# Kernel optimization log

Hardware: AMD Instinct MI355X
Metric: run time of the kernel (lower is better)

The kernel has to match this reference:

```python
import jax, jax.numpy as jnp
import numpy as np

D_MODEL = 1024
N_HEADS = 16
HEAD_DIM = D_MODEL // N_HEADS
B, T = 4, 2048


def setup_inputs() -> dict:
    key = jax.random.key(0)
    k1, k2, k3, k4 = jax.random.split(key, 4)
    x = jax.random.normal(k1, (B, T, D_MODEL), dtype=jnp.float32)
    # bool key-padding mask: True = masked (padded) position
    pad_mask = jax.random.randint(k2, (B, T), 0, 2).astype(jnp.bool_)
    # torch Linear weights: [out_features, in_features], bias=False
    W_qkv = jax.random.normal(k3, (3 * D_MODEL, D_MODEL), dtype=jnp.float32) * (1.0 / np.sqrt(D_MODEL))
    W_proj = jax.random.normal(k4, (D_MODEL, D_MODEL), dtype=jnp.float32) * (1.0 / np.sqrt(D_MODEL))
    return {"x": x, "pad_mask": pad_mask, "W_qkv": W_qkv, "W_proj": W_proj}


def reference(x, pad_mask, W_qkv, W_proj):
    Bv, Tv, C = x.shape
    H, Dh = N_HEADS, HEAD_DIM
    # qkv projection: x @ W_qkv.T -> [B,T,3C], reshape to [B,T,3,H,Dh]
    qkv = jnp.einsum('btc,oc->bto', x, W_qkv).reshape(Bv, Tv, 3, H, Dh)
    q = jnp.transpose(qkv[:, :, 0], (0, 2, 1, 3))  # [B,H,T,Dh]
    k = jnp.transpose(qkv[:, :, 1], (0, 2, 1, 3))
    v = jnp.transpose(qkv[:, :, 2], (0, 2, 1, 3))
    scale = 1.0 / jnp.sqrt(jnp.asarray(Dh, x.dtype))
    attn = jnp.einsum('bhqd,bhkd->bhqk', q, k) * scale  # [B,H,T,T]
    # key-padding mask: broadcast [B,1,1,T]
    attn = jnp.where(pad_mask[:, None, None, :], -jnp.inf, attn)
    attn = jax.nn.softmax(attn, axis=-1)
    out = jnp.einsum('bhqk,bhkd->bhqd', attn, v)  # [B,H,T,Dh]
    out = jnp.transpose(out, (0, 2, 1, 3)).reshape(Bv, Tv, C)
    return jnp.einsum('btc,oc->bto', out, W_proj)
```

## Files before the change

kernel.cpp:

```cpp
#include <hip/hip_runtime.h>
#include <hip/hip_bf16.h>
#include <stdint.h>

typedef __bf16 bf16_t;
typedef __bf16 bf16x8 __attribute__((ext_vector_type(8)));
typedef __bf16 bf16x4 __attribute__((ext_vector_type(4)));
typedef float f32x4 __attribute__((ext_vector_type(4)));

#define DEVFN static __device__ __forceinline__

DEVFN f32x4 mfma16(bf16x8 a, bf16x8 b, f32x4 c) {
  return __builtin_amdgcn_mfma_f32_16x16x32_bf16(a, b, c, 0, 0, 0);
}

#define GLL16(gsrc, ldst) __builtin_amdgcn_global_load_lds( \
    (__attribute__((address_space(1))) void*)(gsrc), \
    (__attribute__((address_space(3))) void*)(ldst), 16, 0, 0)

#define SCALE_Q 0.1803368801111204f

__global__ void prep(const float* __restrict__ x, const float* __restrict__ wqkv,
                     const float* __restrict__ wproj, bf16_t* __restrict__ xb,
                     bf16_t* __restrict__ wqkvb, bf16_t* __restrict__ wprojb,
                     const int* __restrict__ mask, int* __restrict__ tc,
                     int* __restrict__ nk, bf16_t* __restrict__ kb,
                     bf16_t* __restrict__ vtb) {
  const int tid = threadIdx.x;
  if (blockIdx.x < 12288) {
    const int i = blockIdx.x * 256 + tid;
    const float* s;
    bf16_t* d;
    int off;
    if (i < 2097152) { s = x; d = xb; off = i; }
    else if (i < 2097152 + 786432) { s = wqkv; d = wqkvb; off = i - 2097152; }
    else { s = wproj; d = wprojb; off = i - 2883584; }
    f32x4 v = reinterpret_cast<const f32x4*>(s)[off];
    bf16x4 o;
    o[0] = (bf16_t)v[0]; o[1] = (bf16_t)v[1]; o[2] = (bf16_t)v[2]; o[3] = (bf16_t)v[3];
    reinterpret_cast<bf16x4*>(d)[off] = o;
    return;
  }
  const int b = blockIdx.x - 12288;
  const int lane = tid & 63, wv = tid >> 6;
  __shared__ int nk_s;
  const int* mrow = mask + b * 2048;
  if (wv == 0) {
    int base = 0;
    for (int cs = 0; cs < 2048; cs += 64) {
      const int mval = mrow[cs + lane];
      const unsigned long long bal = __ballot(mval == 0);
      const int pre = __popcll(bal & ((1ull << lane) - 1ull));
      if (!mval) tc[b * 2048 + base + pre] = cs + lane;
      base += __popcll(bal);
    }
    if (lane == 0) nk_s = base;
  }
  __syncthreads();
  const int nkb = nk_s;
  if (tid == 0) nk[b] = nkb;
  for (int i = nkb + tid; i < 2048; i += 256) tc[b * 2048 + i] = -1;
  const int ce = (nkb + 63) & ~63;
  for (int hh = wv; hh < 16; hh += 4) {
    const size_t bh = (size_t)(b * 16 + hh);
    for (int r = nkb; r < ce; ++r) {
      kb[(bh * 2048 + r) * 64 + lane] = (bf16_t)0.f;
      vtb[(bh * 64 + lane) * 2048 + r] = (bf16_t)0.f;
    }
  }
}

template <int EPI>
__global__ __launch_bounds__(256, 2)
void gemm_ct(const bf16_t* __restrict__ A, const bf16_t* __restrict__ Bx,
             bf16_t* __restrict__ qb, bf16_t* __restrict__ kb,
             bf16_t* __restrict__ vtb, float* __restrict__ fout,
             const int* __restrict__ tc, const int* __restrict__ nkp) {
  constexpr int K = 1024;
  __shared__ alignas(16) unsigned short At[128 * 64];
  __shared__ alignas(16) unsigned short Bt[128 * 64];
  const int tid = threadIdx.x;
  const int lane = tid & 63, w = tid >> 6;
  const int c = lane & 15, g = lane >> 4;
  const int oBase = blockIdx.x * 128, mBase = blockIdx.y * 128;
  const int wo = (w >> 1) * 64, wm = (w & 1) * 64;

  int nkb = 0;
  bool kv = false;
  if (EPI == 0) {
    nkb = nkp[mBase >> 11];
    kv = (blockIdx.x >= 8);
    if (kv && (mBase & 2047) >= nkb) return;
  }
  int brow[4];
#pragma unroll
  for (int i = 0; i < 4; ++i) {
    const int r = (i * 4 + w) * 8 + (lane >> 3);
    if (EPI == 0 && kv) {
      const int t = tc[(mBase >> 11) * 2048 + (mBase & 2047) + r];
      brow[i] = (mBase & ~2047) + (t < 0 ? 0 : t);
    } else {
      brow[i] = mBase + r;
    }
  }

  f32x4 acc[4][4] = {};

  for (int k0 = 0; k0 < K; k0 += 64) {
#pragma unroll
    for (int i = 0; i < 4; ++i) {
      const int cid = (i * 4 + w) * 64 + lane;
      const int r = cid >> 3;
      const int ss = (cid & 7) ^ (r & 7);
      GLL16(A + (size_t)(oBase + r) * K + k0 + ss * 8, &At[(i * 4 + w) * 512]);
      GLL16(Bx + (size_t)brow[i] * K + k0 + ss * 8, &Bt[(i * 4 + w) * 512]);
    }
    __syncthreads();
    bf16x8 af[4][2], bfr[4][2];
#pragma unroll
    for (int f = 0; f < 4; ++f) {
#pragma unroll
      for (int kc = 0; kc < 2; ++kc) {
        const int ra = wo + f * 16 + c;
        af[f][kc] = *reinterpret_cast<const bf16x8*>(&At[ra * 64 + ((kc * 4 + g) ^ (ra & 7)) * 8]);
        const int rb = wm + f * 16 + c;
        bfr[f][kc] = *reinterpret_cast<const bf16x8*>(&Bt[rb * 64 + ((kc * 4 + g) ^ (rb & 7)) * 8]);
      }
    }
    __builtin_amdgcn_s_setprio(1);
#pragma unroll
    for (int of = 0; of < 4; ++of)
#pragma unroll
      for (int mf = 0; mf < 4; ++mf)
#pragma unroll
        for (int kc = 0; kc < 2; ++kc)
          acc[of][mf] = mfma16(af[of][kc], bfr[mf][kc], acc[of][mf]);
    __builtin_amdgcn_s_setprio(0);
    __syncthreads();
  }

#pragma unroll
  for (int of = 0; of < 4; ++of) {
    const int o0 = oBase + wo + of * 16 + g * 4;
#pragma unroll
    for (int mf = 0; mf < 4; ++mf) {
      const int m = mBase + wm + mf * 16 + c;
      f32x4 v = acc[of][mf];
      if (EPI == 0) {
        if (!kv) {
          v[0] *= SCALE_Q; v[1] *= SCALE_Q; v[2] *= SCALE_Q; v[3] *= SCALE_Q;
          bf16x4 bv;
          bv[0] = (bf16_t)v[0]; bv[1] = (bf16_t)v[1]; bv[2] = (bf16_t)v[2]; bv[3] = (bf16_t)v[3];
          const int rem = o0 & 1023;
          const int h = rem >> 6, d0 = rem & 63;
          const int b = m >> 11, t = m & 2047;
          *reinterpret_cast<bf16x4*>(qb + (((size_t)(b * 16 + h)) * 2048 + t) * 64 + d0) = bv;
        } else {
          const int i = m & 2047;
          if (i < nkb) {
            bf16x4 bv;
            bv[0] = (bf16_t)v[0]; bv[1] = (bf16_t)v[1]; bv[2] = (bf16_t)v[2]; bv[3] = (bf16_t)v[3];
            const int rem = o0 & 1023;
            const int h = rem >> 6, d0 = rem & 63;
            const int b = m >> 11;
            const size_t bh = (size_t)(b * 16 + h);
            if (blockIdx.x < 16) {
              *reinterpret_cast<bf16x4*>(kb + (bh * 2048 + i) * 64 + d0) = bv;
            } else {
#pragma unroll
              for (int j = 0; j < 4; ++j)
                vtb[(bh * 64 + d0 + j) * 2048 + i] = bv[j];
            }
          }
        }
      } else {
        *reinterpret_cast<f32x4*>(fout + (size_t)m * 1024 + o0) = v;
      }
    }
  }
}

__global__ __launch_bounds__(256, 2)
void attn_fwd(const bf16_t* __restrict__ Qg, const bf16_t* __restrict__ Kg,
              const bf16_t* __restrict__ Vtg, const int* __restrict__ nkp,
              bf16_t* __restrict__ aout) {
  constexpr int T = 2048;
  __shared__ alignas(16) unsigned short KtL[2][64 * 64];
  __shared__ alignas(16) unsigned short VtL[2][64 * 64];
  const int tid = threadIdx.x, lane = tid & 63, w = tid >> 6;
  const int c = lane & 15, g = lane >> 4;
  const int bid = blockIdx.x;
  const int xcd = bid & 7, jj = bid >> 3;
  const int bh = xcd * 8 + (jj & 7), qp = jj >> 3;
  const int b = bh >> 4, h = bh & 15;
  const bf16_t* Qh = Qg + (size_t)bh * T * 64;
  const bf16_t* Kh = Kg + (size_t)bh * T * 64;
  const bf16_t* Vh = Vtg + (size_t)bh * 64 * T;
  const int q0 = qp * 256 + w * 64;
  const int nkb = nkp[b];
  const int ntiles = (nkb + 63) >> 6;

  bf16x8 qfr[4][2];
#pragma unroll
  for (int qq = 0; qq < 4; ++qq)
#pragma unroll
    for (int dc = 0; dc < 2; ++dc)
      qfr[qq][dc] = *reinterpret_cast<const bf16x8*>(
          Qh + (size_t)(q0 + qq * 16 + c) * 64 + dc * 32 + g * 8);

  bf16x8 ones;
#pragma unroll
  for (int i = 0; i < 8; ++i) ones[i] = (bf16_t)1.0f;

  f32x4 oacc[4][4] = {};
  float lrun[4] = {0.f, 0.f, 0.f, 0.f};

  auto stage = [&](int t, int bi) {
    const int kt0 = t * 64;
#pragma unroll
    for (int i = 0; i < 2; ++i) {
      const int cid = (i * 4 + w) * 64 + lane;
      const int r = cid >> 3, p = cid & 7;
      const int lk = p ^ ((r & 3) | (((r >> 3) & 1) << 2));
      GLL16(Kh + (size_t)(kt0 + r) * 64 + lk * 8, &KtL[bi][(i * 4 + w) * 512]);
      const int lv = p ^ (r & 7);
      GLL16(Vh + (size_t)r * T + kt0 + lv * 8, &VtL[bi][(i * 4 + w) * 512]);
    }
  };

  stage(0, 0);
  __syncthreads();

  const int fK = (c & 3) | (((c >> 2) & 1) << 2);

  for (int t = 0; t < ntiles; ++t) {
    const int cur = t & 1;
    if (t + 1 < ntiles) stage(t + 1, cur ^ 1);

    bf16x8 kfr[4][2];
#pragma unroll
    for (int kr = 0; kr < 4; ++kr) {
      const int row = (c >> 2) * 8 + (kr & 1) * 4 + (c & 3) + (kr >> 1) * 32;
#pragma unroll
      for (int dc = 0; dc < 2; ++dc)
        kfr[kr][dc] = *reinterpret_cast<const bf16x8*>(
            &KtL[cur][row * 64 + (((dc * 4 + g) ^ fK) * 8)]);
    }

    const bool tail = (t == ntiles - 1) && (nkb & 63) != 0;
    f32x4 bias4[4];
#pragma unroll
    for (int kr = 0; kr < 4; ++kr) {
      if (tail) {
        const int kbase = t * 64 + g * 8 + (kr & 1) * 4 + (kr >> 1) * 32;
#pragma unroll
        for (int j = 0; j < 4; ++j) bias4[kr][j] = (kbase + j < nkb) ? 0.f : -1e30f;
      } else {
        bias4[kr][0] = bias4[kr][1] = bias4[kr][2] = bias4[kr][3] = 0.f;
      }
    }

    bf16x8 pfr[4][2];
#pragma unroll
    for (int qq = 0; qq < 4; ++qq) {
      f32x4 stq[4];
      __builtin_amdgcn_s_setprio(1);
#pragma unroll
      for (int kr = 0; kr < 4; ++kr) {
        f32x4 z = mfma16(kfr[kr][0], qfr[qq][0], bias4[kr]);
        stq[kr] = mfma16(kfr[kr][1], qfr[qq][1], z);
      }
      __builtin_amdgcn_s_setprio(0);
#pragma unroll
      for (int kc = 0; kc < 2; ++kc) {
        bf16x8 p;
#pragma unroll
        for (int j = 0; j < 4; ++j) {
          p[j]     = (bf16_t)__builtin_amdgcn_exp2f(stq[kc * 2 + 0][j]);
          p[4 + j] = (bf16_t)__builtin_amdgcn_exp2f(stq[kc * 2 + 1][j]);
        }
        pfr[qq][kc] = p;
      }
      f32x4 su = {0.f, 0.f, 0.f, 0.f};
      su = mfma16(ones, pfr[qq][0], su);
      su = mfma16(ones, pfr[qq][1], su);
      lrun[qq] += su[0];
    }

    __builtin_amdgcn_s_setprio(1);
#pragma unroll
    for (int df = 0; df < 4; ++df) {
      bf16x8 va[2];
#pragma unroll
      for (int kc = 0; kc < 2; ++kc) {
        const int r = df * 16 + c;
        va[kc] = *reinterpret_cast<const bf16x8*>(
            &VtL[cur][r * 64 + ((kc * 4 + g) ^ (r & 7)) * 8]);
      }
#pragma unroll
      for (int qq = 0; qq < 4; ++qq)
#pragma unroll
        for (int kc = 0; kc < 2; ++kc)
          oacc[df][qq] = mfma16(va[kc], pfr[qq][kc], oacc[df][qq]);
    }
    __builtin_amdgcn_s_setprio(0);
    __syncthreads();
  }

#pragma unroll
  for (int qq = 0; qq < 4; ++qq) {
    const float inv = 1.0f / lrun[qq];
    const int q = q0 + qq * 16 + c;
#pragma unroll
    for (int df = 0; df < 4; ++df) {
      bf16x4 bv;
#pragma unroll
      for (int j = 0; j < 4; ++j) bv[j] = (bf16_t)(oacc[df][qq][j] * inv);
      const int d0 = df * 16 + g * 4;
      *reinterpret_cast<bf16x4*>(aout + ((size_t)(b * 2048 + q)) * 1024 + h * 64 + d0) = bv;
    }
  }
}

extern "C" void kernel_launch(void* const* d_in, const int* in_sizes, int n_in,
                              void* d_out, int out_size, void* d_ws, size_t ws_size,
                              hipStream_t stream) {
  (void)in_sizes; (void)n_in; (void)out_size; (void)ws_size;
  const float* x = (const float*)d_in[0];
  const int* pmask = (const int*)d_in[1];
  const float* wqkv = (const float*)d_in[2];
  const float* wproj = (const float*)d_in[3];
  float* out = (float*)d_out;
  char* ws = (char*)d_ws;

  bf16_t* xb    = (bf16_t*)(ws + 0);
  bf16_t* aob   = (bf16_t*)(ws + 0);
  bf16_t* wqkvb = (bf16_t*)(ws + 16777216);
  bf16_t* wprojb= (bf16_t*)(ws + 23068672);
  bf16_t* Qb    = (bf16_t*)(ws + 25165824);
  bf16_t* Kb    = (bf16_t*)(ws + 41943040);
  bf16_t* Vtb   = (bf16_t*)(ws + 58720256);

  int* tc  = (int*)d_out;
  int* nkp = tc + 4 * 2048;

  prep<<<12292, 256, 0, stream>>>(x, wqkv, wproj, xb, wqkvb, wprojb,
                                  pmask, tc, nkp, Kb, Vtb);

  gemm_ct<0><<<dim3(24, 64), 256, 0, stream>>>(wqkvb, xb, Qb, Kb, Vtb, nullptr, tc, nkp);
  attn_fwd<<<512, 256, 0, stream>>>(Qb, Kb, Vtb, nkp, aob);
  gemm_ct<1><<<dim3(8, 64), 256, 0, stream>>>(wprojb, aob, nullptr, nullptr, nullptr, out,
                                              nullptr, nullptr);
}
```

Before: 156.3 us.

## Rewrite QKV GEMM with 256x256 tiles, double-buffered LDS and XCD-aware block mapping

Replaces the templated 128x128 QKV GEMM with a dedicated 512-thread kernel. It uses 256x256 output tiles and double-buffered LDS, and interleaves the global-to-LDS loads for the next k-tile with MFMA phases under explicit barriers and waitcnts. Blocks are remapped so that neighbouring row tiles land on the same XCD, which should improve L2 reuse. The projection GEMM is split into its own simplified kernel. The aim is to hide load latency and raise arithmetic intensity. The costs are heavier register use (a 4x8 accumulator array), 128KB of LDS per block, and coarser tiles that may hurt occupancy or load balance on padded K/V tiles.

Measured after the change: 170.3 us. 1.09x slower.

```diff
diff --git a/kernel.cpp b/kernel.cpp
--- a/kernel.cpp
+++ b/kernel.cpp
@@ -69,12 +69,146 @@
   }
 }
 
-template <int EPI>
+__global__ __launch_bounds__(512, 2)
+void gemm_qkv8(const bf16_t* __restrict__ A, const bf16_t* __restrict__ Bx,
+               bf16_t* __restrict__ qb, bf16_t* __restrict__ kb,
+               bf16_t* __restrict__ vtb,
+               const int* __restrict__ tc, const int* __restrict__ nkp) {
+  constexpr int K = 1024;
+  constexpr int NT = 16;
+  __shared__ alignas(16) unsigned short At[2][256 * 64];
+  __shared__ alignas(16) unsigned short Bt[2][256 * 64];
+  const int tid = threadIdx.x, lane = tid & 63, w = tid >> 6;
+  const int c = lane & 15, g = lane >> 4;
+  const int bid = blockIdx.x;
+  const int xcd = bid & 7, j = bid >> 3;
+  const int my = xcd * 4 + (j & 3), bx = j >> 2;
+  const int oBase = bx * 256, mBase = my * 256;
+  const int wm = (w >> 2) * 128, wo = (w & 3) * 64;
+  const int which = bx >> 2;
+  const bool kv = which != 0;
+  const int nkb = nkp[mBase >> 11];
+  if (kv && (mBase & 2047) >= nkb) return;
+
+  int brow[4];
+#pragma unroll
+  for (int i = 0; i < 4; ++i) {
+    const int r = (i * 8 + w) * 8 + (lane >> 3);
+    if (kv) {
+      const int t = tc[(mBase >> 11) * 2048 + (mBase & 2047) + r];
+      brow[i] = (mBase & ~2047) + (t < 0 ? 0 : t);
+    } else {
+      brow[i] = mBase + r;
+    }
+  }
+
+  auto stageA = [&](int k0, int bi, int i) {
+    const int cid = (i * 8 + w) * 64 + lane;
+    const int r = cid >> 3, ss = (cid & 7) ^ (r & 7);
+    GLL16(A + (size_t)(oBase + r) * K + k0 + ss * 8, &At[bi][(i * 8 + w) * 512]);
+  };
+  auto stageB = [&](int k0, int bi, int i) {
+    const int cid = (i * 8 + w) * 64 + lane;
+    const int r = cid >> 3, ss = (cid & 7) ^ (r & 7);
+    GLL16(Bx + (size_t)brow[i] * K + k0 + ss * 8, &Bt[bi][(i * 8 + w) * 512]);
+  };
+  auto rdA = [&](int bi, int of, int kc) -> bf16x8 {
+    const int rr = wo + of * 16 + c;
+    return *reinterpret_cast<const bf16x8*>(&At[bi][rr * 64 + (((kc * 4 + g) ^ (rr & 7)) * 8)]);
+  };
+  auto rdB = [&](int bi, int mf, int kc) -> bf16x8 {
+    const int rr = wm + mf * 16 + c;
+    return *reinterpret_cast<const bf16x8*>(&Bt[bi][rr * 64 + (((kc * 4 + g) ^ (rr & 7)) * 8)]);
+  };
+
+  f32x4 acc[4][8] = {};
+
+#pragma unroll
+  for (int i = 0; i < 4; ++i) { stageA(0, 0, i); stageB(0, 0, i); }
+  asm volatile("s_waitcnt vmcnt(0)" ::: "memory");
+  __builtin_amdgcn_s_barrier();
+  __builtin_amdgcn_sched_barrier(0);
+
+#define PHASE(mf0, STA, STB, EXTRA)                                      \
+  {                                                                      \
+    bf16x8 b0k0 = rdB(cur, (mf0), 0), b0k1 = rdB(cur, (mf0), 1);         \
+    bf16x8 b1k0 = rdB(cur, (mf0) + 1, 0), b1k1 = rdB(cur, (mf0) + 1, 1); \
+    if (more) { STA; STB; }                                              \
+    __builtin_amdgcn_s_barrier();                                        \
+    asm volatile("s_waitcnt lgkmcnt(0)" ::: "memory");                   \
+    __builtin_amdgcn_sched_barrier(0);                                   \
+    __builtin_amdgcn_s_setprio(1);                                       \
+    _Pragma("unroll")                                                    \
+    for (int of = 0; of < 4; ++of) {                                     \
+      acc[of][(mf0)]     = mfma16(af[of][0], b0k0, acc[of][(mf0)]);      \
+      acc[of][(mf0)]     = mfma16(af[of][1], b0k1, acc[of][(mf0)]);      \
+      acc[of][(mf0) + 1] = mfma16(af[of][0], b1k0, acc[of][(mf0) + 1]);  \
+      acc[of][(mf0) + 1] = mfma16(af[of][1], b1k1, acc[of][(mf0) + 1]);  \
+    }                                                                    \
+    __builtin_amdgcn_s_setprio(0);                                       \
+    EXTRA;                                                               \
+    __builtin_amdgcn_s_barrier();                                        \
+    __builtin_amdgcn_sched_barrier(0);                                   \
+  }
+
+  for (int t = 0; t < NT; ++t) {
+    const int cur = t & 1, nxt = cur ^ 1;
+    const int k0n = (t + 1) * 64;
+    const bool more = t < NT - 1;
+    bf16x8 af[4][2];
+#pragma unroll
+    for (int of = 0; of < 4; ++of) {
+      af[of][0] = rdA(cur, of, 0);
+      af[of][1] = rdA(cur, of, 1);
+    }
+    PHASE(0, stageA(k0n, nxt, 0), stageB(k0n, nxt, 0), ;)
+    PHASE(2, stageA(k0n, nxt, 1), stageB(k0n, nxt, 1), ;)
+    PHASE(4, stageA(k0n, nxt, 2), stageB(k0n, nxt, 2), ;)
+    PHASE(6, stageA(k0n, nxt, 3), stageB(k0n, nxt, 3),
+          asm volatile("s_waitcnt vmcnt(0)" ::: "memory"))
+  }
+#undef PHASE
+
+#pragma unroll
+  for (int of = 0; of < 4; ++of) {
+    const int o0 = oBase + wo + of * 16 + g * 4;
+#pragma unroll
+    for (int mf = 0; mf < 8; ++mf) {
+      const int m = mBase + wm + mf * 16 + c;
+      f32x4 v = acc[of][mf];
+      if (which == 0) {
+        v[0] *= SCALE_Q; v[1] *= SCALE_Q; v[2] *= SCALE_Q; v[3] *= SCALE_Q;
+        bf16x4 bv;
+        bv[0] = (bf16_t)v[0]; bv[1] = (bf16_t)v[1]; bv[2] = (bf16_t)v[2]; bv[3] = (bf16_t)v[3];
+        const int rem = o0 & 1023;
+        const int h = rem >> 6, d0 = rem & 63;
+        const int b = m >> 11, t = m & 2047;
+        *reinterpret_cast<bf16x4*>(qb + (((size_t)(b * 16 + h)) * 2048 + t) * 64 + d0) = bv;
+      } else {
+        const int i = m & 2047;
+        if (i < nkb) {
+          bf16x4 bv;
+          bv[0] = (bf16_t)v[0]; bv[1] = (bf16_t)v[1]; bv[2] = (bf16_t)v[2]; bv[3] = (bf16_t)v[3];
+          const int rem = o0 & 1023;
+          const int h = rem >> 6, d0 = rem & 63;
+          const int b = m >> 11;
+          const size_t bh = (size_t)(b * 16 + h);
+          if (which == 1) {
+            *reinterpret_cast<bf16x4*>(kb + (bh * 2048 + i) * 64 + d0) = bv;
+          } else {
+#pragma unroll
+            for (int jj = 0; jj < 4; ++jj)
+              vtb[(bh * 64 + d0 + jj) * 2048 + i] = bv[jj];
+          }
+        }
+      }
+    }
+  }
+}
+
 __global__ __launch_bounds__(256, 2)
-void gemm_ct(const bf16_t* __restrict__ A, const bf16_t* __restrict__ Bx,
-             bf16_t* __restrict__ qb, bf16_t* __restrict__ kb,
-             bf16_t* __restrict__ vtb, float* __restrict__ fout,
-             const int* __restrict__ tc, const int* __restrict__ nkp) {
+void gemm_proj(const bf16_t* __restrict__ A, const bf16_t* __restrict__ Bx,
+               float* __restrict__ fout) {
   constexpr int K = 1024;
   __shared__ alignas(16) unsigned short At[128 * 64];
   __shared__ alignas(16) unsigned short Bt[128 * 64];
@@ -84,25 +218,6 @@
   const int oBase = blockIdx.x * 128, mBase = blockIdx.y * 128;
   const int wo = (w >> 1) * 64, wm = (w & 1) * 64;
 
-  int nkb = 0;
-  bool kv = false;
-  if (EPI == 0) {
-    nkb = nkp[mBase >> 11];
-    kv = (blockIdx.x >= 8);
-    if (kv && (mBase & 2047) >= nkb) return;
-  }
-  int brow[4];
-#pragma unroll
-  for (int i = 0; i < 4; ++i) {
-    const int r = (i * 4 + w) * 8 + (lane >> 3);
-    if (EPI == 0 && kv) {
-      const int t = tc[(mBase >> 11) * 2048 + (mBase & 2047) + r];
-      brow[i] = (mBase & ~2047) + (t < 0 ? 0 : t);
-    } else {
-      brow[i] = mBase + r;
-    }
-  }
-
   f32x4 acc[4][4] = {};
 
   for (int k0 = 0; k0 < K; k0 += 64) {
@@ -112,7 +227,7 @@
       const int r = cid >> 3;
       const int ss = (cid & 7) ^ (r & 7);
       GLL16(A + (size_t)(oBase + r) * K + k0 + ss * 8, &At[(i * 4 + w) * 512]);
-      GLL16(Bx + (size_t)brow[i] * K + k0 + ss * 8, &Bt[(i * 4 + w) * 512]);
+      GLL16(Bx + (size_t)(mBase + r) * K + k0 + ss * 8, &Bt[(i * 4 + w) * 512]);
     }
     __syncthreads();
     bf16x8 af[4][2], bfr[4][2];
@@ -144,37 +259,7 @@
 #pragma unroll
     for (int mf = 0; mf < 4; ++mf) {
       const int m = mBase + wm + mf * 16 + c;
-      f32x4 v = acc[of][mf];
-      if (EPI == 0) {
-        if (!kv) {
-          v[0] *= SCALE_Q; v[1] *= SCALE_Q; v[2] *= SCALE_Q; v[3] *= SCALE_Q;
-          bf16x4 bv;
-          bv[0] = (bf16_t)v[0]; bv[1] = (bf16_t)v[1]; bv[2] = (bf16_t)v[2]; bv[3] = (bf16_t)v[3];
-          const int rem = o0 & 1023;
-          const int h = rem >> 6, d0 = rem & 63;
-          const int b = m >> 11, t = m & 2047;
-          *reinterpret_cast<bf16x4*>(qb + (((size_t)(b * 16 + h)) * 2048 + t) * 64 + d0) = bv;
-        } else {
-          const int i = m & 2047;
-          if (i < nkb) {
-            bf16x4 bv;
-            bv[0] = (bf16_t)v[0]; bv[1] = (bf16_t)v[1]; bv[2] = (bf16_t)v[2]; bv[3] = (bf16_t)v[3];
-            const int rem = o0 & 1023;
-            const int h = rem >> 6, d0 = rem & 63;
-            const int b = m >> 11;
-            const size_t bh = (size_t)(b * 16 + h);
-            if (blockIdx.x < 16) {
-              *reinterpret_cast<bf16x4*>(kb + (bh * 2048 + i) * 64 + d0) = bv;
-            } else {
-#pragma unroll
-              for (int j = 0; j < 4; ++j)
-                vtb[(bh * 64 + d0 + j) * 2048 + i] = bv[j];
-            }
-          }
-        }
-      } else {
-        *reinterpret_cast<f32x4*>(fout + (size_t)m * 1024 + o0) = v;
-      }
+      *reinterpret_cast<f32x4*>(fout + (size_t)m * 1024 + o0) = acc[of][mf];
     }
   }
 }
@@ -346,8 +431,7 @@
   prep<<<12292, 256, 0, stream>>>(x, wqkv, wproj, xb, wqkvb, wprojb,
                                   pmask, tc, nkp, Kb, Vtb);
 
-  gemm_ct<0><<<dim3(24, 64), 256, 0, stream>>>(wqkvb, xb, Qb, Kb, Vtb, nullptr, tc, nkp);
+  gemm_qkv8<<<384, 512, 0, stream>>>(wqkvb, xb, Qb, Kb, Vtb, tc, nkp);
   attn_fwd<<<512, 256, 0, stream>>>(Qb, Kb, Vtb, nkp, aob);
-  gemm_ct<1><<<dim3(8, 64), 256, 0, stream>>>(wprojb, aob, nullptr, nullptr, nullptr, out,
-                                              nullptr, nullptr);
-}
+  gemm_proj<<<dim3(8, 64), 256, 0, stream>>>(wprojb, aob, out);
+}
```
